# Kernel optimization log

Hardware: AMD Instinct MI355X
Metric: run time of the kernel (lower is better)

The kernel has to match this reference:

```python
import jax, jax.numpy as jnp
import numpy as np

BN_EPS = 1e-5


def conv1x1(x, w, b):
    # x: [B,C,H,W], w: [O,C], b: [O] -> [B,O,H,W]
    return jnp.einsum('bchw,oc->bohw', x, w) + b[None, :, None, None]


def setup_inputs() -> dict:
    key = jax.random.key(0)
    ks = jax.random.split(key, 11)
    B, C, H, W = 8, 1024, 64, 32
    hid = 64  # C * rd_ratio (1/16)
    s = 0.02
    return {
        'x': jax.random.normal(ks[0], (B, C, H, W), dtype=jnp.float32),
        'theta_w': jax.random.normal(ks[1], (hid, C), dtype=jnp.float32) * s,
        'theta_b': jax.random.normal(ks[2], (hid,), dtype=jnp.float32) * s,
        'phi_w': jax.random.normal(ks[3], (hid, C), dtype=jnp.float32) * s,
        'phi_b': jax.random.normal(ks[4], (hid,), dtype=jnp.float32) * s,
        'g_w': jax.random.normal(ks[5], (hid, C), dtype=jnp.float32) * s,
        'g_b': jax.random.normal(ks[6], (hid,), dtype=jnp.float32) * s,
        'w_w': jax.random.normal(ks[7], (C, hid), dtype=jnp.float32) * s,
        'w_b': jax.random.normal(ks[8], (C,), dtype=jnp.float32) * s,
        'bn_gamma': jax.random.normal(ks[9], (C,), dtype=jnp.float32) * 0.1 + 1.0,
        'bn_beta': jax.random.normal(ks[10], (C,), dtype=jnp.float32) * 0.1,
    }


def reference(x, theta_w, theta_b, phi_w, phi_b, g_w, g_b, w_w, w_b, bn_gamma, bn_beta):
    B, C, H, W = x.shape
    hid = theta_w.shape[0]
    N = H * W
    theta = conv1x1(x, theta_w, theta_b).reshape(B, hid, N).transpose(0, 2, 1)  # [B,N,d]
    phi = conv1x1(x, phi_w, phi_b).reshape(B, hid, N)                           # [B,d,N]
    g = conv1x1(x, g_w, g_b).reshape(B, hid, N).transpose(0, 2, 1)              # [B,N,d]
    f = jnp.einsum('bnd,bdm->bnm', theta, phi) / N                              # [B,N,N]
    y = jnp.einsum('bnm,bmd->bnd', f, g)                                        # [B,N,d]
    y = y.transpose(0, 2, 1).reshape(B, hid, H, W)
    wy = conv1x1(y, w_w, w_b)                                                   # [B,C,H,W]
    # BatchNorm2d in training mode: batch statistics over (B,H,W), biased variance
    mean = wy.mean(axis=(0, 2, 3), keepdims=True)
    var = wy.var(axis=(0, 2, 3), keepdims=True)
    norm = (wy - mean) * jax.lax.rsqrt(var + BN_EPS)
    out = norm * bn_gamma[None, :, None, None] + bn_beta[None, :, None, None]
    return out + x
```

## Files before the change

### kernel.cpp

```cpp
#include <hip/hip_runtime.h>

#define B_    8
#define C_    1024
#define HID   64
#define N_    2048
#define RTOT  192

typedef __attribute__((ext_vector_type(8))) short   bf16x8;
typedef __attribute__((ext_vector_type(4))) unsigned short ush4;
typedef __attribute__((ext_vector_type(4))) float   f32x4;
typedef __attribute__((ext_vector_type(16))) float  f32x16;

#define WSB_WBF   ((size_t)0)
#define WSB_TPG   ((size_t)393216)
#define WSB_THT   ((size_t)6684672)
#define WSB_M     ((size_t)8781824)
#define WSB_G     ((size_t)8912896)
#define WSB_S     ((size_t)9043968)
#define WSB_WMBF  ((size_t)9046016)
#define WSB_SC    ((size_t)10094592)
#define WSB_SH    ((size_t)10098688)

#define MGS_FLOATS (2 * B_ * HID * HID + B_ * HID)

static __device__ __forceinline__ unsigned short f2bf(float f) {
    union { float f; unsigned u; } v; v.f = f;
    unsigned r = v.u + 0x7fffu + ((v.u >> 16) & 1u);
    return (unsigned short)(r >> 16);
}
static __device__ __forceinline__ float bf2f(unsigned short h) {
    union { unsigned u; float f; } v; v.u = ((unsigned)h) << 16;
    return v.f;
}

static __device__ __forceinline__ void gload16(const unsigned short* g, unsigned short* l) {
    __builtin_amdgcn_global_load_lds(
        (const __attribute__((address_space(1))) unsigned int*)g,
        (__attribute__((address_space(3))) unsigned int*)l, 16, 0, 0);
}

__global__ __launch_bounds__(256) void wcvt(
    const float* __restrict__ tw, const float* __restrict__ pw,
    const float* __restrict__ gw, unsigned short* __restrict__ wbf,
    float* __restrict__ mgs)
{
    int idx = blockIdx.x * 256 + threadIdx.x;
    if (blockIdx.x < 258) {
        int z = blockIdx.x * 256 + threadIdx.x;
        if (z < MGS_FLOATS) mgs[z] = 0.f;
    }
    int r = idx >> 10, k = idx & 1023;
    float v = (r < 64) ? tw[(size_t)r * 1024 + k]
            : (r < 128) ? pw[(size_t)(r - 64) * 1024 + k]
                        : gw[(size_t)(r - 128) * 1024 + k];
    wbf[idx] = f2bf(v);
}

__global__ __launch_bounds__(256, 2) void projx_mfma(
    const float* __restrict__ x, const unsigned short* __restrict__ wbf,
    const float* __restrict__ tb, const float* __restrict__ pb,
    const float* __restrict__ gb, unsigned short* __restrict__ tpgbf,
    unsigned short* __restrict__ thT)
{
    const int b = blockIdx.y, n0 = blockIdx.x * 32;
    const int t = threadIdx.x, w = t >> 6, L = t & 63;
    const int wn = w & 1, wc = w >> 1;
    const int lr = L & 15, q = L >> 4;

    __shared__ unsigned short Abuf[2][32][64];
    __shared__ unsigned short Bbuf[2][192][64];

    f32x4 acc[6] = {};

    const int n4 = t & 7;
    const int g  = t >> 3;
    const float* xbase = x + (size_t)b * C_ * N_ + n0 + n4 * 4;

    f32x4 vr[2];
    auto loadX = [&](int s) {
        const float* p = xbase + (size_t)(64 * s + 2 * g) * N_;
        vr[0] = *(const f32x4*)(p);
        vr[1] = *(const f32x4*)(p + N_);
    };
    auto writeA = [&](int cb) {
#pragma unroll
        for (int rrow = 0; rrow < 4; rrow++) {
            int n  = 4 * n4 + rrow;
            int sw = (n ^ (n >> 3)) & 7;
            int ss = (g >> 2) ^ sw;
            unsigned val = (unsigned)f2bf(vr[0][rrow]) | ((unsigned)f2bf(vr[1][rrow]) << 16);
            ((unsigned*)&Abuf[cb][n][0])[ss * 4 + (g & 3)] = val;
        }
    };
    auto stageB = [&](int cb, int s) {
        const int k0 = 64 * s;
#pragma unroll
        for (int i = 0; i < 6; i++) {
            int o = (i * 256 + t) * 16;
            int row = o >> 7, slot = (o >> 4) & 7, ss = slot ^ (row & 7);
            gload16(wbf + ((size_t)row) * 1024 + k0 + ss * 8,
                    &Bbuf[cb][0][0] + o / 2);
        }
    };

    const int swB = lr & 7;
    const int nfa = wn * 16 + lr;
    const int swA = (nfa ^ (nfa >> 3)) & 7;
    auto compute = [&](int cur) {
#pragma unroll
        for (int ksub = 0; ksub < 2; ksub++) {
            bf16x8 Af = *(const bf16x8*)&Abuf[cur][nfa][((ksub * 4 + q) ^ swA) * 8];
            bf16x8 Bf[6];
#pragma unroll
            for (int j = 0; j < 6; j++)
                Bf[j] = *(const bf16x8*)&Bbuf[cur][wc * 96 + j * 16 + lr]
                                              [((ksub * 4 + q) ^ swB) * 8];
#pragma unroll
            for (int j = 0; j < 6; j++)
                acc[j] = __builtin_amdgcn_mfma_f32_16x16x32_bf16(
                    Af, Bf[j], acc[j], 0, 0, 0);
        }
    };

    loadX(0);
    asm volatile("s_waitcnt vmcnt(0)" ::: "memory");
    writeA(0);
    stageB(0, 0);
    loadX(1);
    asm volatile("s_waitcnt vmcnt(2)" ::: "memory");
    asm volatile("s_waitcnt lgkmcnt(0)" ::: "memory");
    __builtin_amdgcn_s_barrier();

    int cur = 0;
    for (int s = 0; s < 16; s++) {
        if (s < 15) {
            writeA(cur ^ 1);
            stageB(cur ^ 1, s + 1);
        }
        if (s < 14) loadX(s + 2);
        compute(cur);
        if (s < 14)
            asm volatile("s_waitcnt vmcnt(2)" ::: "memory");
        else
            asm volatile("s_waitcnt vmcnt(0)" ::: "memory");
        asm volatile("s_waitcnt lgkmcnt(0)" ::: "memory");
        if (s < 15) __builtin_amdgcn_s_barrier();
        cur ^= 1;
    }

#pragma unroll
    for (int j = 0; j < 6; j++) {
        int rcol = 96 * wc + 16 * j + lr;
        float bias = (rcol < 64) ? tb[rcol]
                   : (rcol < 128) ? pb[rcol - 64] : gb[rcol - 128];
        ush4 o;
#pragma unroll
        for (int rr = 0; rr < 4; rr++) o[rr] = f2bf(acc[j][rr] + bias);
        int nglob = n0 + wn * 16 + q * 4;
        *(ush4*)(tpgbf + ((size_t)b * RTOT + rcol) * N_ + nglob) = o;
        if (rcol < HID) {
#pragma unroll
            for (int rr = 0; rr < 4; rr++)
                thT[((size_t)b * N_ + nglob + rr) * HID + rcol] = o[rr];
        }
    }
}

__global__ __launch_bounds__(256) void gram_mfma(
    const unsigned short* __restrict__ tpgbf, float* __restrict__ Mm,
    float* __restrict__ Gg, float* __restrict__ S)
{
    const int kc = blockIdx.x, p = blockIdx.y, b = blockIdx.z;
    const int t = threadIdx.x, w = t >> 6, L = t & 63;
    const int lr = L & 15, q = L >> 4;
    const unsigned short* base = tpgbf + (size_t)b * RTOT * N_;
    const unsigned short* Arow = base + (p ? 0 : (size_t)64 * N_);
    const unsigned short* Brow = base + (p ? 0 : (size_t)128 * N_);
    const unsigned short* ap = Arow + ((size_t)(16 * w + lr)) * N_ + kc * 128 + q * 8;
    const unsigned short* bp = Brow + ((size_t)lr) * N_ + kc * 128 + q * 8;

    bf16x8 ones;
#pragma unroll
    for (int j = 0; j < 8; j++) ones[j] = (short)0x3F80;

    f32x4 acc[4] = {};
    f32x4 accs = {};
#pragma unroll
    for (int it = 0; it < 4; ++it) {
        const int kn = it * 32;
        bf16x8 a = *(const bf16x8*)(ap + kn);
#pragma unroll
        for (int g = 0; g < 4; g++) {
            bf16x8 bb = *(const bf16x8*)(bp + (size_t)g * 16 * N_ + kn);
            acc[g] = __builtin_amdgcn_mfma_f32_16x16x32_bf16(a, bb, acc[g], 0, 0, 0);
        }
        if (p) accs = __builtin_amdgcn_mfma_f32_16x16x32_bf16(a, ones, accs, 0, 0, 0);
    }
    float* outp = (p ? Gg : Mm) + (size_t)b * HID * HID;
#pragma unroll
    for (int g = 0; g < 4; g++)
#pragma unroll
        for (int r = 0; r < 4; r++) {
            int row = 16 * w + q * 4 + r, col = 16 * g + lr;
            atomicAdd(outp + row * HID + col, acc[g][r]);
        }
    if (p && lr == 0) {
#pragma unroll
        for (int r = 0; r < 4; r++)
            atomicAdd(S + b * HID + 16 * w + q * 4 + r, accs[r]);
    }
}

__global__ __launch_bounds__(512, 1) void wmstat(
    const float* __restrict__ ww, const float* __restrict__ Mm,
    const float* __restrict__ S, const float* __restrict__ G,
    const float* __restrict__ wb, const float* __restrict__ gamma,
    const float* __restrict__ beta, unsigned short* __restrict__ wmbf,
    float* __restrict__ scale, float* __restrict__ shift2)
{
    const int c0 = blockIdx.x * 4;
    const int t = threadIdx.x;
    const int b = t >> 6, lane = t & 63;

    f32x4 mrow[16], grow[16];
    {
        const f32x4* mr4 = (const f32x4*)(Mm + ((size_t)b * HID + lane) * HID);
        const f32x4* gr4 = (const f32x4*)(G  + (size_t)b * HID * HID + (size_t)lane * HID);
#pragma unroll
        for (int i = 0; i < 16; i++) mrow[i] = mr4[i];
#pragma unroll
        for (int i = 0; i < 16; i++) grow[i] = gr4[i];
    }
    const float sv = S[b * HID + lane];

    __shared__ float vsh[8][64];
    __shared__ float red[4][16];

#pragma unroll
    for (int ci = 0; ci < 4; ci++) {
        const int c = c0 + ci;
        const float wbc = wb[c];
        const float* wr = ww + (size_t)c * HID;

        float acc = 0.f;
#pragma unroll
        for (int d = 0; d < 16; d++) {
            f32x4 w4 = *(const f32x4*)(wr + 4 * d);
            acc += w4[0] * mrow[d][0] + w4[1] * mrow[d][1]
                 + w4[2] * mrow[d][2] + w4[3] * mrow[d][3];
        }
        unsigned short us = f2bf(acc * (1.0f / N_));
        wmbf[((size_t)b * C_ + c) * HID + lane] = us;
        float v = bf2f(us);
        float t1 = v * sv;
        for (int off = 32; off; off >>= 1) t1 += __shfl_down(t1, off);
        t1 = __shfl(t1, 0);

        __syncthreads();
        vsh[b][lane] = v;
        __syncthreads();

        const f32x4* vb4 = (const f32x4*)&vsh[b][0];
        float inner = 0.f;
#pragma unroll
        for (int fo = 0; fo < 16; fo++) {
            f32x4 vv = vb4[fo];
            inner = fmaf(grow[fo][0], vv[0], inner);
            inner = fmaf(grow[fo][1], vv[1], inner);
            inner = fmaf(grow[fo][2], vv[2], inner);
            inner = fmaf(grow[fo][3], vv[3], inner);
        }
        float qq = v * inner;
        for (int off = 32; off; off >>= 1) qq += __shfl_down(qq, off);
        qq = __shfl(qq, 0);

        if (lane == 0) {
            red[ci][b] = t1;
            red[ci][8 + b] = qq + 2.f * wbc * t1;
        }
    }
    __syncthreads();
    if (t < 4) {
        const int c = c0 + t;
        float asum = 0.f, asq = 0.f;
#pragma unroll
        for (int i = 0; i < 8; i++) { asum += red[t][i]; asq += red[t][8 + i]; }
        const float wbc = wb[c];
        const float cnt = (float)B_ * (float)N_;
        const float inv = 1.0f / cnt;
        float mean = (asum + cnt * wbc) * inv;
        float e2   = (asq + cnt * wbc * wbc) * inv;
        float var  = e2 - mean * mean;
        float sc   = gamma[c] * rsqrtf(var + 1e-5f);
        scale[c]  = sc;
        shift2[c] = beta[c] - mean * sc + sc * wbc;
    }
}

__global__ __launch_bounds__(256) void finalk_mfma(
    const unsigned short* __restrict__ wmbf, const unsigned short* __restrict__ thT,
    const float* __restrict__ x, const float* __restrict__ scale,
    const float* __restrict__ shift2, float* __restrict__ out)
{
    const int b = blockIdx.z, c0 = blockIdx.y * 32, n0b = blockIdx.x * 128;
    const int t = threadIdx.x, w = t >> 6, L = t & 63;
    const int n0 = n0b + w * 32;
    const int rr = L & 31, kh = L >> 5;

    const unsigned short* apw = wmbf + ((size_t)b * C_ + c0 + rr) * HID + kh * 8;
    const unsigned short* bpt = thT + ((size_t)b * N_ + n0 + rr) * HID + kh * 8;

    float xv[16];
#pragma unroll
    for (int r = 0; r < 16; r++) {
        int cl = (r & 3) + 8 * (r >> 2) + 4 * kh;
        xv[r] = x[((size_t)b * C_ + c0 + cl) * N_ + n0 + rr];
    }

    f32x16 acc = {};
#pragma unroll
    for (int kk = 0; kk < 4; kk++) {
        bf16x8 A  = *(const bf16x8*)(apw + kk * 16);
        bf16x8 Bv = *(const bf16x8*)(bpt + kk * 16);
        acc = __builtin_amdgcn_mfma_f32_32x32x16_bf16(A, Bv, acc, 0, 0, 0);
    }

#pragma unroll
    for (int r = 0; r < 16; r++) {
        int cl = (r & 3) + 8 * (r >> 2) + 4 * kh;
        int c  = c0 + cl;
        size_t off = ((size_t)b * C_ + c) * N_ + n0 + rr;
        out[off] = fmaf(scale[c], acc[r], shift2[c]) + xv[r];
    }
}

extern "C" void kernel_launch(void* const* d_in, const int* in_sizes, int n_in,
                              void* d_out, int out_size, void* d_ws, size_t ws_size,
                              hipStream_t stream)
{
    const float* x  = (const float*)d_in[0];
    const float* tw = (const float*)d_in[1];
    const float* tb = (const float*)d_in[2];
    const float* pw = (const float*)d_in[3];
    const float* pb = (const float*)d_in[4];
    const float* gw = (const float*)d_in[5];
    const float* gb = (const float*)d_in[6];
    const float* ww = (const float*)d_in[7];
    const float* wb = (const float*)d_in[8];
    const float* gamma = (const float*)d_in[9];
    const float* beta  = (const float*)d_in[10];
    float* out = (float*)d_out;

    char* ws = (char*)d_ws;
    unsigned short* wbf   = (unsigned short*)(ws + WSB_WBF);
    unsigned short* tpgbf = (unsigned short*)(ws + WSB_TPG);
    unsigned short* thT   = (unsigned short*)(ws + WSB_THT);
    float* Mm   = (float*)(ws + WSB_M);
    float* Gg   = (float*)(ws + WSB_G);
    float* S    = (float*)(ws + WSB_S);
    unsigned short* wmbf = (unsigned short*)(ws + WSB_WMBF);
    float* scl  = (float*)(ws + WSB_SC);
    float* shf  = (float*)(ws + WSB_SH);

    wcvt<<<dim3(RTOT * 1024 / 256), 256, 0, stream>>>(tw, pw, gw, wbf, Mm);
    projx_mfma<<<dim3(64, B_), 256, 0, stream>>>(x, wbf, tb, pb, gb, tpgbf, thT);
    gram_mfma<<<dim3(16, 2, B_), 256, 0, stream>>>(tpgbf, Mm, Gg, S);
    wmstat<<<C_ / 4, 512, 0, stream>>>(ww, Mm, S, Gg, wb, gamma, beta, wmbf, scl, shf);
    finalk_mfma<<<dim3(16, 32, B_), 256, 0, stream>>>(wmbf, thT, x, scl, shf, out);
}
```

Before: 193.2 us.

## Fuse gram matrix computation into projection kernel via shared memory tile

```diff
diff --git a/kernel.cpp b/kernel.cpp
--- a/kernel.cpp
+++ b/kernel.cpp
@@ -12,7 +12,6 @@
 typedef __attribute__((ext_vector_type(16))) float  f32x16;
 
 #define WSB_WBF   ((size_t)0)
-#define WSB_TPG   ((size_t)393216)
 #define WSB_THT   ((size_t)6684672)
 #define WSB_M     ((size_t)8781824)
 #define WSB_G     ((size_t)8912896)
@@ -59,16 +58,21 @@
 __global__ __launch_bounds__(256, 2) void projx_mfma(
     const float* __restrict__ x, const unsigned short* __restrict__ wbf,
     const float* __restrict__ tb, const float* __restrict__ pb,
-    const float* __restrict__ gb, unsigned short* __restrict__ tpgbf,
-    unsigned short* __restrict__ thT)
+    const float* __restrict__ gb, unsigned short* __restrict__ thT,
+    float* __restrict__ Mm, float* __restrict__ Gg, float* __restrict__ S)
 {
     const int b = blockIdx.y, n0 = blockIdx.x * 32;
     const int t = threadIdx.x, w = t >> 6, L = t & 63;
     const int wn = w & 1, wc = w >> 1;
     const int lr = L & 15, q = L >> 4;
 
-    __shared__ unsigned short Abuf[2][32][64];
-    __shared__ unsigned short Bbuf[2][192][64];
+    typedef unsigned short AbufT[2][32][64];
+    typedef unsigned short BbufT[2][192][64];
+    typedef unsigned short PT[192][40];
+    __shared__ __align__(16) char smem[57344];
+    AbufT& Abuf = *reinterpret_cast<AbufT*>(smem);
+    BbufT& Bbuf = *reinterpret_cast<BbufT*>(smem + 8192);
+    PT&    Pls  = *reinterpret_cast<PT*>(smem);
 
     f32x4 acc[6] = {};
 
@@ -148,6 +152,8 @@
         cur ^= 1;
     }
 
+    __syncthreads();
+
 #pragma unroll
     for (int j = 0; j < 6; j++) {
         int rcol = 96 * wc + 16 * j + lr;
@@ -156,58 +162,48 @@
         ush4 o;
 #pragma unroll
         for (int rr = 0; rr < 4; rr++) o[rr] = f2bf(acc[j][rr] + bias);
-        int nglob = n0 + wn * 16 + q * 4;
-        *(ush4*)(tpgbf + ((size_t)b * RTOT + rcol) * N_ + nglob) = o;
+        int nl = 16 * wn + q * 4;
+        *(ush4*)&Pls[rcol][nl] = o;
         if (rcol < HID) {
+            int nglob = n0 + nl;
 #pragma unroll
             for (int rr = 0; rr < 4; rr++)
                 thT[((size_t)b * N_ + nglob + rr) * HID + rcol] = o[rr];
         }
     }
-}
-
-__global__ __launch_bounds__(256) void gram_mfma(
-    const unsigned short* __restrict__ tpgbf, float* __restrict__ Mm,
-    float* __restrict__ Gg, float* __restrict__ S)
-{
-    const int kc = blockIdx.x, p = blockIdx.y, b = blockIdx.z;
-    const int t = threadIdx.x, w = t >> 6, L = t & 63;
-    const int lr = L & 15, q = L >> 4;
-    const unsigned short* base = tpgbf + (size_t)b * RTOT * N_;
-    const unsigned short* Arow = base + (p ? 0 : (size_t)64 * N_);
-    const unsigned short* Brow = base + (p ? 0 : (size_t)128 * N_);
-    const unsigned short* ap = Arow + ((size_t)(16 * w + lr)) * N_ + kc * 128 + q * 8;
-    const unsigned short* bp = Brow + ((size_t)lr) * N_ + kc * 128 + q * 8;
+    __syncthreads();
 
     bf16x8 ones;
 #pragma unroll
     for (int j = 0; j < 8; j++) ones[j] = (short)0x3F80;
 
-    f32x4 acc[4] = {};
-    f32x4 accs = {};
-#pragma unroll
-    for (int it = 0; it < 4; ++it) {
-        const int kn = it * 32;
-        bf16x8 a = *(const bf16x8*)(ap + kn);
-#pragma unroll
-        for (int g = 0; g < 4; g++) {
-            bf16x8 bb = *(const bf16x8*)(bp + (size_t)g * 16 * N_ + kn);
-            acc[g] = __builtin_amdgcn_mfma_f32_16x16x32_bf16(a, bb, acc[g], 0, 0, 0);
-        }
-        if (p) accs = __builtin_amdgcn_mfma_f32_16x16x32_bf16(a, ones, accs, 0, 0, 0);
-    }
-    float* outp = (p ? Gg : Mm) + (size_t)b * HID * HID;
-#pragma unroll
-    for (int g = 0; g < 4; g++)
-#pragma unroll
-        for (int r = 0; r < 4; r++) {
-            int row = 16 * w + q * 4 + r, col = 16 * g + lr;
-            atomicAdd(outp + row * HID + col, acc[g][r]);
-        }
-    if (p && lr == 0) {
-#pragma unroll
-        for (int r = 0; r < 4; r++)
-            atomicAdd(S + b * HID + 16 * w + q * 4 + r, accs[r]);
+    bf16x8 Aphi = *(const bf16x8*)&Pls[64 + 16 * w + lr][q * 8];
+    bf16x8 Ath  = *(const bf16x8*)&Pls[16 * w + lr][q * 8];
+
+    f32x4 aM[4] = {}, aG[4] = {}, aS = {};
+#pragma unroll
+    for (int gt = 0; gt < 4; gt++) {
+        bf16x8 Bg = *(const bf16x8*)&Pls[128 + 16 * gt + lr][q * 8];
+        bf16x8 Bt = *(const bf16x8*)&Pls[16 * gt + lr][q * 8];
+        aM[gt] = __builtin_amdgcn_mfma_f32_16x16x32_bf16(Aphi, Bg, aM[gt], 0, 0, 0);
+        aG[gt] = __builtin_amdgcn_mfma_f32_16x16x32_bf16(Ath,  Bt, aG[gt], 0, 0, 0);
+    }
+    aS = __builtin_amdgcn_mfma_f32_16x16x32_bf16(Ath, ones, aS, 0, 0, 0);
+
+    float* Mb = Mm + (size_t)b * HID * HID;
+    float* Gb = Gg + (size_t)b * HID * HID;
+#pragma unroll
+    for (int gt = 0; gt < 4; gt++)
+#pragma unroll
+        for (int rr = 0; rr < 4; rr++) {
+            int row = 16 * w + 4 * q + rr, col = 16 * gt + lr;
+            atomicAdd(Mb + row * HID + col, aM[gt][rr]);
+            atomicAdd(Gb + row * HID + col, aG[gt][rr]);
+        }
+    if (lr == 0) {
+#pragma unroll
+        for (int rr = 0; rr < 4; rr++)
+            atomicAdd(S + b * HID + 16 * w + 4 * q + rr, aS[rr]);
     }
 }
 
@@ -353,7 +349,6 @@
 
     char* ws = (char*)d_ws;
     unsigned short* wbf   = (unsigned short*)(ws + WSB_WBF);
-    unsigned short* tpgbf = (unsigned short*)(ws + WSB_TPG);
     unsigned short* thT   = (unsigned short*)(ws + WSB_THT);
     float* Mm   = (float*)(ws + WSB_M);
     float* Gg   = (float*)(ws + WSB_G);
@@ -363,8 +358,7 @@
     float* shf  = (float*)(ws + WSB_SH);
 
     wcvt<<<dim3(RTOT * 1024 / 256), 256, 0, stream>>>(tw, pw, gw, wbf, Mm);
-    projx_mfma<<<dim3(64, B_), 256, 0, stream>>>(x, wbf, tb, pb, gb, tpgbf, thT);
-    gram_mfma<<<dim3(16, 2, B_), 256, 0, stream>>>(tpgbf, Mm, Gg, S);
+    projx_mfma<<<dim3(64, B_), 256, 0, stream>>>(x, wbf, tb, pb, gb, thT, Mm, Gg, S);
     wmstat<<<C_ / 4, 512, 0, stream>>>(ww, Mm, S, Gg, wb, gamma, beta, wmbf, scl, shf);
     finalk_mfma<<<dim3(16, 32, B_), 256, 0, stream>>>(wmbf, thT, x, scl, shf, out);
 }
```

After: 194.6 us. Within noise of the previous version (+0.7%).
